# Kernel tuning notes

Measured on AMD Instinct MI355X. Metric: run time of the kernel, lower is better.

The kernel has to match this reference:

```python
import jax, jax.numpy as jnp
import numpy as np
import math

HEADS = 16
DIMS = 1024
SEQ_LEN = 2048
RANK_K = 128
BATCH = 8


def setup_inputs() -> dict:
    key = jax.random.key(0)
    ks = jax.random.split(key, 14)
    dh_std = 1.0 / math.sqrt(DIMS)
    proj_std = 1.0 / math.sqrt(RANK_K)
    inp = {
        "q": jax.random.normal(ks[0], (BATCH, SEQ_LEN, DIMS), jnp.float32),
        "k": jax.random.normal(ks[1], (BATCH, SEQ_LEN, DIMS), jnp.float32),
        "v": jax.random.normal(ks[2], (BATCH, SEQ_LEN, DIMS), jnp.float32),
        # nn.Linear weights [out, in], bias [out]
        "Wq": jax.random.uniform(ks[3], (DIMS, DIMS), jnp.float32, -dh_std, dh_std),
        "bq": jax.random.uniform(ks[4], (DIMS,), jnp.float32, -dh_std, dh_std),
        "Wk": jax.random.uniform(ks[5], (DIMS, DIMS), jnp.float32, -dh_std, dh_std),
        "bk": jax.random.uniform(ks[6], (DIMS,), jnp.float32, -dh_std, dh_std),
        "Wv": jax.random.uniform(ks[7], (DIMS, DIMS), jnp.float32, -dh_std, dh_std),
        "bv": jax.random.uniform(ks[8], (DIMS,), jnp.float32, -dh_std, dh_std),
        # Linformer low-rank projections [seq_length, k], uniform(-1/sqrt(k), 1/sqrt(k))
        "proj_k": jax.random.uniform(ks[9], (SEQ_LEN, RANK_K), jnp.float32, -proj_std, proj_std),
        "proj_v": jax.random.uniform(ks[10], (SEQ_LEN, RANK_K), jnp.float32, -proj_std, proj_std),
        "Wo": jax.random.uniform(ks[11], (DIMS, DIMS), jnp.float32, -dh_std, dh_std),
        "bo": jax.random.uniform(ks[12], (DIMS,), jnp.float32, -dh_std, dh_std),
    }
    return inp


def reference(q, k, v, Wq, bq, Wk, bk, Wv, bv, proj_k, proj_v, Wo, bo):
    B, N, D = q.shape
    H = HEADS
    dh = D // H
    Kr = proj_k.shape[1]

    kp = k @ Wk.T + bk                       # [B, N, D]
    # faithful to original: plain reshape (view), NOT a head-split transpose
    qp = (q @ Wq.T + bq).reshape(B, H, N, dh)  # [B, H, N, dh]
    vp = v @ Wv.T + bv                       # [B, N, D]

    pk = jnp.einsum('bnd,nk->bkd', kp, proj_k[:N])  # [B, Kr, D]
    pv = jnp.einsum('bnd,nk->bkd', vp, proj_v[:N])  # [B, Kr, D]
    pk = pk.reshape(B, Kr, H, dh).transpose(0, 2, 1, 3)  # [B, H, Kr, dh]
    pv = pv.reshape(B, Kr, H, dh).transpose(0, 2, 1, 3)  # [B, H, Kr, dh]

    # scores [B,H,N,Kr] -> transposed to [B,H,Kr,N]; softmax over N (seq) axis
    scores = jnp.einsum('bhnd,bhkd->bhkn', qp, pk) / math.sqrt(dh)
    attn = jax.nn.softmax(scores, axis=-1)   # [B, H, Kr, N]
    out = jnp.einsum('bhkn,bhkd->bhnd', attn, pv)  # [B, H, N, dh]
    out = out.transpose(0, 2, 1, 3).reshape(B, N, D)
    return out @ Wo.T + bo
```

## Files before the change

### kernel.cpp

```cpp
#include <hip/hip_runtime.h>

typedef unsigned short u16;
typedef unsigned int   u32;
typedef __attribute__((ext_vector_type(4))) float fx4;
typedef __attribute__((ext_vector_type(8))) __bf16 bf16x8;
typedef __attribute__((ext_vector_type(8))) unsigned short us8;
typedef __attribute__((ext_vector_type(2))) unsigned int u32x2;

__device__ __forceinline__ u16 f2bf(float x){
  u32 u = __builtin_bit_cast(u32, x);
  u += 0x7fffu + ((u >> 16) & 1u);
  return (u16)(u >> 16);
}
__device__ __forceinline__ float b2f(u16 h){
  u32 u = ((u32)h) << 16;
  return __builtin_bit_cast(float, u);
}
__device__ __forceinline__ void gld16(const void* g, void* l){
  __builtin_amdgcn_global_load_lds(
      (const __attribute__((address_space(1))) u32*)g,
      (__attribute__((address_space(3))) u32*)l, 16, 0, 0);
}
__device__ __forceinline__ void xcd_remap(u32& bx, u32& by, u32& bz){
  u32 nx = gridDim.x, ny = gridDim.y, nz = gridDim.z;
  u32 nwg = nx * ny * nz;
  u32 orig = (blockIdx.z * ny + blockIdx.y) * nx + blockIdx.x;
  u32 lid = (orig & 7u) * (nwg >> 3) + (orig >> 3);
  bx = lid % nx;
  u32 rem = lid / nx;
  by = rem % ny;
  bz = rem / ny;
}

__global__ __launch_bounds__(256) void k_f2bfAll(const float* __restrict__ w0,
                                                 const float* __restrict__ w1,
                                                 const float* __restrict__ w2,
                                                 const float* __restrict__ w3,
                                                 const float* __restrict__ q,
                                                 u16* __restrict__ wout,
                                                 u16* __restrict__ qout,
                                                 float* __restrict__ zbuf){
  if (blockIdx.x == 0 && blockIdx.y == 0) zbuf[threadIdx.x] = 0.f;
  const int y = blockIdx.y;
  const float* src;
  u16* dst;
  if (y < 4){
    src = y == 0 ? w0 : y == 1 ? w1 : y == 2 ? w2 : w3;
    dst = wout + (long)y * 1048576;
  } else {
    src = q + (long)(y - 4) * 1048576;
    dst = qout + (long)(y - 4) * 1048576;
  }
  int i = blockIdx.x * 256 + threadIdx.x;
  const int stride = gridDim.x * 256;
  for (; i < 131072; i += stride){
    const float4* p = (const float4*)src + (long)i * 2;
    float4 a = p[0], b = p[1];
    us8 o = { f2bf(a.x), f2bf(a.y), f2bf(a.z), f2bf(a.w),
              f2bf(b.x), f2bf(b.y), f2bf(b.z), f2bf(b.w) };
    *((us8*)dst + i) = o;
  }
}

__global__ __launch_bounds__(256) void k_tconvKV(const float* __restrict__ ksrc,
                                                 const float* __restrict__ vsrc,
                                                 u16* __restrict__ kT){
  const int z = blockIdx.z;
  const float* in = (z >= 8 ? vsrc : ksrc) + (long)(z & 7) * 2097152;
  u16* out = kT + (long)(z >> 3) * 16777216 + (long)(z & 7) * 2097152;
  const int c0 = blockIdx.x * 64, r0 = blockIdx.y * 64;
  __shared__ u16 tile[64][66];
  const int t = threadIdx.x;
  const int cc = t & 63, wq = t >> 6;
  #pragma unroll
  for (int i = 0; i < 16; ++i){
    int rr = i * 4 + wq;
    tile[rr][cc] = f2bf(in[(long)(r0 + rr) * 1024 + c0 + cc]);
  }
  __syncthreads();
  const int oc0 = t >> 5, jb = (t & 31) * 2;
  #pragma unroll
  for (int i = 0; i < 8; ++i){
    int oc = oc0 + i * 8;
    u32 pk2 = (u32)tile[jb][oc] | ((u32)tile[jb + 1][oc] << 16);
    *(u32*)(out + (long)(c0 + oc) * 2048 + r0 + jb) = pk2;
  }
}

__global__ __launch_bounds__(256) void k_tconvP(const float* __restrict__ pjk,
                                                const float* __restrict__ pjv,
                                                u16* __restrict__ projT,
                                                float* __restrict__ ssum){
  const int z = blockIdx.z;
  const float* in = z ? pjv : pjk;
  u16* out = projT + z * 262144;
  float* colsum = ssum + z * 128;
  const int c0 = blockIdx.x * 64, r0 = blockIdx.y * 64;
  __shared__ u16 tile[64][66];
  __shared__ float red[256];
  const int t = threadIdx.x;
  const int cc = t & 63, wq = t >> 6;
  float part = 0.f;
  #pragma unroll
  for (int i = 0; i < 16; ++i){
    int rr = i * 4 + wq;
    float v = in[(long)(r0 + rr) * 128 + c0 + cc];
    tile[rr][cc] = f2bf(v);
    part += v;
  }
  red[t] = part;
  __syncthreads();
  if (t < 64){
    float s = red[t] + red[t + 64] + red[t + 128] + red[t + 192];
    atomicAdd(&colsum[c0 + t], s);
  }
  __syncthreads();
  const int oc0 = t >> 5, jb = (t & 31) * 2;
  #pragma unroll
  for (int i = 0; i < 8; ++i){
    int oc = oc0 + i * 8;
    u32 pk2 = (u32)tile[jb][oc] | ((u32)tile[jb + 1][oc] << 16);
    *(u32*)(out + (long)(c0 + oc) * 2048 + r0 + jb) = pk2;
  }
}

template<int BM, int BN, int MODE, int EPI, typename OutT>
__global__ __launch_bounds__(256) void k_gemm(
    const u16* __restrict__ A, int lda, long sAz,
    const u16* __restrict__ B, int ldb, long sBz,
    OutT* __restrict__ C, int ldc, long sCz,
    int K, const float* __restrict__ bias, const float* __restrict__ srow, float scale)
{
  constexpr int BK = 64;
  constexpr int FM = BM / 32, FN = BN / 32;
  __shared__ u16 ldsA[BM * BK];
  __shared__ u16 ldsB[BN * BK];
  u32 bx, by, bz;
  xcd_remap(bx, by, bz);
  const long z = bz;
  if constexpr (MODE == 0){ A += z * sAz; B += z * sBz; C += z * sCz; }
  if constexpr (MODE == 3){ long p = z >> 3, bb = z & 7;
                            A += p * 262144; B += p * 16777216 + bb * 2097152;
                            C += p * 1048576 + bb * 131072; }
  const int t = threadIdx.x;
  const int lane = t & 63;
  const int w = t >> 6, wm = w >> 1, wn = w & 1;
  const int r15 = lane & 15, g = lane >> 4;
  const int m0 = by * BM, n0 = bx * BN;
  fx4 acc[FM][FN] = {};
  constexpr int CA = BM * BK / (8 * 256);
  constexpr int CB = BN * BK / (8 * 256);
  for (int kt = 0; kt < K; kt += BK){
    #pragma unroll
    for (int i = 0; i < CA; ++i){
      int ch = i * 256 + t, row = ch >> 3, cc = ch & 7;
      gld16(A + (long)(m0 + row) * lda + kt + cc * 8, (char*)ldsA + ch * 16);
    }
    #pragma unroll
    for (int i = 0; i < CB; ++i){
      int ch = i * 256 + t, row = ch >> 3, cc = ch & 7;
      gld16(B + (long)(n0 + row) * ldb + kt + cc * 8, (char*)ldsB + ch * 16);
    }
    __syncthreads();
    #pragma unroll
    for (int ks = 0; ks < 2; ++ks){
      bf16x8 af[FM], bfv[FN];
      #pragma unroll
      for (int mf = 0; mf < FM; ++mf)
        af[mf] = *(const bf16x8*)&ldsA[(wm * (BM/2) + mf * 16 + r15) * BK + ks * 32 + g * 8];
      #pragma unroll
      for (int nf = 0; nf < FN; ++nf)
        bfv[nf] = *(const bf16x8*)&ldsB[(wn * (BN/2) + nf * 16 + r15) * BK + ks * 32 + g * 8];
      #pragma unroll
      for (int mf = 0; mf < FM; ++mf)
        #pragma unroll
        for (int nf = 0; nf < FN; ++nf)
          acc[mf][nf] = __builtin_amdgcn_mfma_f32_16x16x32_bf16(af[mf], bfv[nf], acc[mf][nf], 0, 0, 0);
    }
    __syncthreads();
  }
  #pragma unroll
  for (int mf = 0; mf < FM; ++mf){
    #pragma unroll
    for (int nf = 0; nf < FN; ++nf){
      const int row0 = m0 + wm * (BM/2) + mf * 16 + g * 4;
      const int col  = n0 + wn * (BN/2) + nf * 16 + r15;
      float vv[4];
      #pragma unroll
      for (int r = 0; r < 4; ++r){
        float v = acc[mf][nf][r];
        if constexpr (EPI == 1) v += bias[col];
        vv[r] = v;
      }
      #pragma unroll
      for (int r = 0; r < 4; ++r){
        if constexpr (sizeof(OutT) == 2) C[(long)(row0 + r) * ldc + col] = (OutT)f2bf(vv[r]);
        else                             C[(long)(row0 + r) * ldc + col] = (OutT)vv[r];
      }
    }
  }
}

__global__ __launch_bounds__(256) void k_pkpv(
    const u16* __restrict__ ck, const u16* __restrict__ Wk_bf,
    const u16* __restrict__ Wv_bf, const float* __restrict__ bk,
    const float* __restrict__ bv, const float* __restrict__ ssum,
    u16* __restrict__ pk, u16* __restrict__ pvT)
{
  constexpr int BM = 64, BN = 64, BK = 64;
  __shared__ u16 ldsA[BM * BK];
  __shared__ u16 ldsB[BN * BK];
  u32 bx, by, bz;
  xcd_remap(bx, by, bz);
  const int half = bz >> 3, b = bz & 7;
  const u16* A = ck + half * 1048576 + b * 131072;
  const u16* B = half ? Wv_bf : Wk_bf;
  const float* bias = half ? bv : bk;
  const float* srow = ssum + half * 128;
  const float scale = half ? 1.f : 0.125f;
  const int t = threadIdx.x;
  const int lane = t & 63;
  const int w = t >> 6, wm = w >> 1, wn = w & 1;
  const int r15 = lane & 15, g = lane >> 4;
  const int m0 = by * BM, n0 = bx * BN;
  fx4 acc[2][2] = {};
  for (int kt = 0; kt < 1024; kt += BK){
    #pragma unroll
    for (int i = 0; i < 2; ++i){
      int ch = i * 256 + t, row = ch >> 3, cc = ch & 7;
      gld16(A + (long)(m0 + row) * 1024 + kt + cc * 8, (char*)ldsA + ch * 16);
    }
    #pragma unroll
    for (int i = 0; i < 2; ++i){
      int ch = i * 256 + t, row = ch >> 3, cc = ch & 7;
      gld16(B + (long)(n0 + row) * 1024 + kt + cc * 8, (char*)ldsB + ch * 16);
    }
    __syncthreads();
    #pragma unroll
    for (int ks = 0; ks < 2; ++ks){
      bf16x8 af[2], bfv[2];
      #pragma unroll
      for (int mf = 0; mf < 2; ++mf)
        af[mf] = *(const bf16x8*)&ldsA[(wm * 32 + mf * 16 + r15) * BK + ks * 32 + g * 8];
      #pragma unroll
      for (int nf = 0; nf < 2; ++nf)
        bfv[nf] = *(const bf16x8*)&ldsB[(wn * 32 + nf * 16 + r15) * BK + ks * 32 + g * 8];
      #pragma unroll
      for (int mf = 0; mf < 2; ++mf)
        #pragma unroll
        for (int nf = 0; nf < 2; ++nf)
          acc[mf][nf] = __builtin_amdgcn_mfma_f32_16x16x32_bf16(af[mf], bfv[nf], acc[mf][nf], 0, 0, 0);
    }
    __syncthreads();
  }
  #pragma unroll
  for (int mf = 0; mf < 2; ++mf){
    #pragma unroll
    for (int nf = 0; nf < 2; ++nf){
      const int row0 = m0 + wm * 32 + mf * 16 + g * 4;
      const int col  = n0 + wn * 32 + nf * 16 + r15;
      float vv[4];
      #pragma unroll
      for (int r = 0; r < 4; ++r)
        vv[r] = (acc[mf][nf][r] + srow[row0 + r] * bias[col]) * scale;
      if (!half){
        #pragma unroll
        for (int r = 0; r < 4; ++r)
          pk[b * 131072 + (long)(row0 + r) * 1024 + col] = f2bf(vv[r]);
      } else {
        u32 lo = (u32)f2bf(vv[0]) | ((u32)f2bf(vv[1]) << 16);
        u32 hi = (u32)f2bf(vv[2]) | ((u32)f2bf(vv[3]) << 16);
        u32x2 pk2 = { lo, hi };
        *(u32x2*)(pvT + b * 131072 + (long)col * 128 + row0) = pk2;
      }
    }
  }
}

template<int EPI, typename OutT>
__global__ __launch_bounds__(512, 1) void k_gemm256(
    const u16* __restrict__ A, int lda,
    const u16* __restrict__ B, int ldb,
    OutT* __restrict__ C, int ldc,
    int K, const float* __restrict__ bias)
{
  constexpr int BM = 256, BN = 128, BK = 64;
  __shared__ u16 ldsA[3][BM * BK];
  __shared__ u16 ldsB[3][BN * BK];
  u32 bx, by, bz;
  xcd_remap(bx, by, bz);
  const int m0 = by * BM, n0 = bx * BN;
  const int t = threadIdx.x;
  const int lane = t & 63, w = t >> 6;
  const int wm = w >> 1, wn = w & 1;
  const int r15 = lane & 15, g = lane >> 4;
  const int NT = K >> 6;

  auto stageA = [&](int kt, int buf){
    #pragma unroll
    for (int j = 0; j < 4; ++j){
      int ch = j * 512 + t, row = ch >> 3, cc = ch & 7;
      gld16(A + (long)(m0 + row) * lda + kt + ((cc ^ (row & 7)) * 8),
            (char*)ldsA[buf] + ch * 16);
    }
  };
  auto stageB = [&](int kt, int buf){
    #pragma unroll
    for (int j = 0; j < 2; ++j){
      int ch = j * 512 + t, row = ch >> 3, cc = ch & 7;
      gld16(B + (long)(n0 + row) * ldb + kt + ((cc ^ (row & 7)) * 8),
            (char*)ldsB[buf] + ch * 16);
    }
  };

  stageA(0, 0); stageB(0, 0);
  if (NT > 1){
    stageA(BK, 1); stageB(BK, 1);
    asm volatile("s_waitcnt vmcnt(6)" ::: "memory");
  } else {
    asm volatile("s_waitcnt vmcnt(0)" ::: "memory");
  }
  __builtin_amdgcn_s_barrier();
  asm volatile("" ::: "memory");

  fx4 acc[4][4] = {};
  for (int tt = 0; tt < NT; ++tt){
    const u16* bA = ldsA[tt % 3];
    const u16* bB = ldsB[tt % 3];
    const int sbuf = (tt + 2) % 3;
    const bool pf = (tt + 2 < NT);
    bf16x8 af[2][4], bf[2][2];
    #pragma unroll
    for (int ks = 0; ks < 2; ++ks)
      #pragma unroll
      for (int mf = 0; mf < 4; ++mf)
        af[ks][mf] = *(const bf16x8*)((const char*)bA +
            (wm * 64 + mf * 16 + r15) * 128 + (((ks * 4 + g) ^ (r15 & 7)) * 16));
    #pragma unroll
    for (int ks = 0; ks < 2; ++ks)
      #pragma unroll
      for (int nf = 0; nf < 2; ++nf)
        bf[ks][nf] = *(const bf16x8*)((const char*)bB +
            (wn * 64 + nf * 16 + r15) * 128 + (((ks * 4 + g) ^ (r15 & 7)) * 16));
    if (pf) stageA((tt + 2) * BK, sbuf);
    asm volatile("" ::: "memory");
    __builtin_amdgcn_s_barrier();
    asm volatile("" ::: "memory");
    __builtin_amdgcn_s_setprio(1);
    #pragma unroll
    for (int ks = 0; ks < 2; ++ks)
      #pragma unroll
      for (int mf = 0; mf < 4; ++mf)
        #pragma unroll
        for (int nf = 0; nf < 2; ++nf)
          acc[mf][nf] = __builtin_amdgcn_mfma_f32_16x16x32_bf16(af[ks][mf], bf[ks][nf], acc[mf][nf], 0, 0, 0);
    __builtin_amdgcn_s_setprio(0);
    asm volatile("" ::: "memory");
    __builtin_amdgcn_s_barrier();
    asm volatile("" ::: "memory");
    bf16x8 bf2[2][2];
    #pragma unroll
    for (int ks = 0; ks < 2; ++ks)
      #pragma unroll
      for (int nf = 0; nf < 2; ++nf)
        bf2[ks][nf] = *(const bf16x8*)((const char*)bB +
            (wn * 64 + (nf + 2) * 16 + r15) * 128 + (((ks * 4 + g) ^ (r15 & 7)) * 16));
    if (pf) stageB((tt + 2) * BK, sbuf);
    __builtin_amdgcn_s_setprio(1);
    #pragma unroll
    for (int ks = 0; ks < 2; ++ks)
      #pragma unroll
      for (int mf = 0; mf < 4; ++mf)
        #pragma unroll
        for (int nf = 0; nf < 2; ++nf)
          acc[mf][nf + 2] = __builtin_amdgcn_mfma_f32_16x16x32_bf16(af[ks][mf], bf2[ks][nf], acc[mf][nf + 2], 0, 0, 0);
    __builtin_amdgcn_s_setprio(0);
    if (pf)                { asm volatile("s_waitcnt vmcnt(6)" ::: "memory"); }
    else if (tt + 1 < NT)  { asm volatile("s_waitcnt vmcnt(0)" ::: "memory"); }
    asm volatile("" ::: "memory");
    __builtin_amdgcn_s_barrier();
    asm volatile("" ::: "memory");
  }

  #pragma unroll
  for (int mf = 0; mf < 4; ++mf)
    #pragma unroll
    for (int nf = 0; nf < 4; ++nf){
      const int row0 = m0 + wm * 64 + mf * 16 + g * 4;
      const int col  = n0 + wn * 64 + nf * 16 + r15;
      float bcol = 0.f;
      if constexpr (EPI == 1) bcol = bias[col];
      #pragma unroll
      for (int r = 0; r < 4; ++r){
        float vv = acc[mf][nf][r] + bcol;
        if constexpr (sizeof(OutT) == 2) C[(long)(row0 + r) * ldc + col] = (OutT)f2bf(vv);
        else                             C[(long)(row0 + r) * ldc + col] = (OutT)vv;
      }
    }
}

__global__ __launch_bounds__(512) void k_stats(const u16* __restrict__ pk,
                                               const u16* __restrict__ qp,
                                               float* __restrict__ zpart){
  const int hf = blockIdx.x, z = blockIdx.y;
  const int b = z >> 4, h = z & 15;
  const u16* pkh = pk + b * 131072 + h * 64;
  const u16* qph = qp + (long)z * 131072;
  __shared__ u16 pkL[128 * 64];
  __shared__ float zred[8][128];
  const int t = threadIdx.x, lane = t & 63, w = t >> 6;
  const int r15 = lane & 15, g = lane >> 4;
  #pragma unroll
  for (int i = 0; i < 2; ++i){
    int ch = i * 512 + t, row = ch >> 3, cc = ch & 7;
    int csrc = cc ^ (row & 7);
    gld16(pkh + (long)row * 1024 + csrc * 8, (char*)pkL + ch * 16);
  }
  __syncthreads();
  float zacc[8][4] = {};
  for (int c = 0; c < 4; ++c){
    const int n0 = hf * 1024 + w * 128 + c * 32;
    fx4 acc[8][2] = {};
    #pragma unroll
    for (int ks = 0; ks < 2; ++ks){
      bf16x8 bq[2];
      #pragma unroll
      for (int nf = 0; nf < 2; ++nf)
        bq[nf] = *(const bf16x8*)(qph + (long)(n0 + nf * 16 + r15) * 64 + ks * 32 + g * 8);
      #pragma unroll
      for (int mf = 0; mf < 8; ++mf){
        int row = mf * 16 + r15;
        int x = (ks * 4 + g) ^ (row & 7);
        bf16x8 a = *(const bf16x8*)((const char*)pkL + row * 128 + x * 16);
        #pragma unroll
        for (int nf = 0; nf < 2; ++nf)
          acc[mf][nf] = __builtin_amdgcn_mfma_f32_16x16x32_bf16(a, bq[nf], acc[mf][nf], 0, 0, 0);
      }
    }
    #pragma unroll
    for (int mf = 0; mf < 8; ++mf)
      #pragma unroll
      for (int nf = 0; nf < 2; ++nf)
        #pragma unroll
        for (int r = 0; r < 4; ++r)
          zacc[mf][r] += __expf(acc[mf][nf][r]);
  }
  #pragma unroll
  for (int mf = 0; mf < 8; ++mf)
    #pragma unroll
    for (int r = 0; r < 4; ++r){
      float v = zacc[mf][r];
      v += __shfl_xor(v, 1); v += __shfl_xor(v, 2);
      v += __shfl_xor(v, 4); v += __shfl_xor(v, 8);
      zacc[mf][r] = v;
    }
  if (r15 == 0){
    #pragma unroll
    for (int mf = 0; mf < 8; ++mf)
      #pragma unroll
      for (int r = 0; r < 4; ++r)
        zred[w][mf * 16 + g * 4 + r] = zacc[mf][r];
  }
  __syncthreads();
  if (t < 128){
    float s = 0.f;
    #pragma unroll
    for (int w2 = 0; w2 < 8; ++w2) s += zred[w2][t];
    zpart[hf * 16384 + (long)z * 128 + t] = s;
  }
}

__global__ __launch_bounds__(256) void k_attn(const u16* __restrict__ pk,
                                              const u16* __restrict__ qp,
                                              const u16* __restrict__ pvT,
                                              const float* __restrict__ zpart,
                                              u16* __restrict__ outh){
  u32 bx, by, bz;
  xcd_remap(bx, by, bz);
  const int z = by, nb = bx;
  const int b = z >> 4, h = z & 15;
  const u16* pkh = pk  + b * 131072 + h * 64;
  const u16* qph = qp  + (long)z * 131072;
  const u16* pvh = pvT + b * 131072 + h * 8192;
  __shared__ u16 pkL[128 * 64];
  __shared__ u16 ptL[4][32 * 132];
  __shared__ float zL[128];
  const int t = threadIdx.x, lane = t & 63, w = t >> 6;
  const int r15 = lane & 15, g = lane >> 4;
  #pragma unroll
  for (int i = 0; i < 4; ++i){
    int ch = i * 256 + t, row = ch >> 3, cc = ch & 7;
    int csrc = cc ^ (row & 7);
    gld16(pkh + (long)row * 1024 + csrc * 8, (char*)pkL + ch * 16);
  }
  if (t < 128)
    zL[t] = 1.0f / (zpart[(long)z * 128 + t] + zpart[16384 + (long)z * 128 + t]);
  __syncthreads();
  const int n0 = nb * 128 + w * 32;
  fx4 acc[8][2] = {};
  #pragma unroll
  for (int ks = 0; ks < 2; ++ks){
    bf16x8 bq[2];
    #pragma unroll
    for (int nf = 0; nf < 2; ++nf)
      bq[nf] = *(const bf16x8*)(qph + (long)(n0 + nf * 16 + r15) * 64 + ks * 32 + g * 8);
    #pragma unroll
    for (int mf = 0; mf < 8; ++mf){
      int row = mf * 16 + r15;
      int x = (ks * 4 + g) ^ (row & 7);
      bf16x8 a = *(const bf16x8*)((const char*)pkL + row * 128 + x * 16);
      #pragma unroll
      for (int nf = 0; nf < 2; ++nf)
        acc[mf][nf] = __builtin_amdgcn_mfma_f32_16x16x32_bf16(a, bq[nf], acc[mf][nf], 0, 0, 0);
    }
  }
  u16* pt = ptL[w];
  #pragma unroll
  for (int mf = 0; mf < 8; ++mf){
    const int kb = mf * 16 + g * 4;
    const float z0 = zL[kb], z1 = zL[kb + 1], z2 = zL[kb + 2], z3 = zL[kb + 3];
    #pragma unroll
    for (int nf = 0; nf < 2; ++nf){
      const int nl = nf * 16 + r15;
      u32 lo = (u32)f2bf(__expf(acc[mf][nf][0]) * z0) |
               ((u32)f2bf(__expf(acc[mf][nf][1]) * z1) << 16);
      u32 hi = (u32)f2bf(__expf(acc[mf][nf][2]) * z2) |
               ((u32)f2bf(__expf(acc[mf][nf][3]) * z3) << 16);
      u32x2 pkd = { lo, hi };
      *(u32x2*)(pt + nl * 132 + kb) = pkd;
    }
  }
  fx4 o[2][4] = {};
  #pragma unroll
  for (int ks = 0; ks < 4; ++ks){
    bf16x8 bv[4];
    #pragma unroll
    for (int nf = 0; nf < 4; ++nf)
      bv[nf] = *(const bf16x8*)(pvh + (long)(nf * 16 + r15) * 128 + ks * 32 + g * 8);
    #pragma unroll
    for (int mf = 0; mf < 2; ++mf){
      bf16x8 pa = *(const bf16x8*)(pt + (mf * 16 + r15) * 132 + ks * 32 + g * 8);
      #pragma unroll
      for (int nf = 0; nf < 4; ++nf)
        o[mf][nf] = __builtin_amdgcn_mfma_f32_16x16x32_bf16(pa, bv[nf], o[mf][nf], 0, 0, 0);
    }
  }
  u16* og = outh + ((long)b * 2048 + n0) * 1024 + h * 64;
  #pragma unroll
  for (int mf = 0; mf < 2; ++mf)
    #pragma unroll
    for (int nf = 0; nf < 4; ++nf)
      #pragma unroll
      for (int r = 0; r < 4; ++r){
        int nl = mf * 16 + g * 4 + r;
        og[(long)nl * 1024 + nf * 16 + r15] = f2bf(o[mf][nf][r]);
      }
}

extern "C" void kernel_launch(void* const* d_in, const int* in_sizes, int n_in,
                              void* d_out, int out_size, void* d_ws, size_t ws_size,
                              hipStream_t stream)
{
  const float* q   = (const float*)d_in[0];
  const float* k   = (const float*)d_in[1];
  const float* v   = (const float*)d_in[2];
  const float* Wq  = (const float*)d_in[3];
  const float* bq  = (const float*)d_in[4];
  const float* Wk  = (const float*)d_in[5];
  const float* bk  = (const float*)d_in[6];
  const float* Wv  = (const float*)d_in[7];
  const float* bv  = (const float*)d_in[8];
  const float* pjk = (const float*)d_in[9];
  const float* pjv = (const float*)d_in[10];
  const float* Wo  = (const float*)d_in[11];
  const float* bo  = (const float*)d_in[12];

  if (ws_size < 152044544u) return;

  char* ws = (char*)d_ws;
  u16*  q_bf  = (u16*)(ws + 0);
  u16*  kT    = (u16*)(ws + 33554432);
  u16*  vT    = (u16*)(ws + 67108864);
  u16*  W_bf  = (u16*)(ws + 100663296);
  u16*  projT = (u16*)(ws + 109051904);
  float* sk   = (float*)(ws + 110100480);
  u16*  qp    = (u16*)(ws + 110101504);
  u16*  ck    = (u16*)(ws + 143655936);
  u16*  pk    = (u16*)(ws + 147850240);
  u16*  pvT   = (u16*)(ws + 149947392);
  float* zpart = (float*)(ws + 33554432);
  u16*  outh  = (u16*)(ws + 0);
  u16*  Wq_bf = W_bf, *Wk_bf = W_bf + 1048576, *Wv_bf = W_bf + 2097152, *Wo_bf = W_bf + 3145728;

  k_f2bfAll<<<dim3(128,20), 256, 0, stream>>>(Wq, Wk, Wv, Wo, q, W_bf, q_bf, sk);
  k_tconvP<<<dim3(2,32,2), 256, 0, stream>>>(pjk, pjv, projT, sk);
  k_tconvKV<<<dim3(16,32,16), 256, 0, stream>>>(k, v, kT);

  k_gemm256<1,u16><<<dim3(8,64), 512, 0, stream>>>(
      q_bf,1024, Wq_bf,1024, qp,1024, 1024, bq);
  k_gemm<128,64,3,0,u16><<<dim3(16,1,16), 256, 0, stream>>>(
      projT,2048,0, kT,2048,0, ck,1024,0, 2048, nullptr, nullptr, 1.f);
  k_pkpv<<<dim3(16,2,16), 256, 0, stream>>>(ck, Wk_bf, Wv_bf, bk, bv, sk, pk, pvT);
  k_stats<<<dim3(2,128), 512, 0, stream>>>(pk, qp, zpart);
  k_attn<<<dim3(16,128), 256, 0, stream>>>(pk, qp, pvT, zpart, outh);
  k_gemm256<1,float><<<dim3(8,64), 512, 0, stream>>>(
      outh,1024, Wo_bf,1024, (float*)d_out,1024, 1024, bo);
}
```

Measured before the change: 263.8 us.

## Enlarge GEMM tile to 256x256 with double-buffered staggered LDS staging

```diff
diff --git a/kernel.cpp b/kernel.cpp
--- a/kernel.cpp
+++ b/kernel.cpp
@@ -278,74 +278,84 @@
 }
 
 template<int EPI, typename OutT>
-__global__ __launch_bounds__(512, 1) void k_gemm256(
+__global__ __launch_bounds__(512, 1) void k_gemm256b(
     const u16* __restrict__ A, int lda,
     const u16* __restrict__ B, int ldb,
     OutT* __restrict__ C, int ldc,
     int K, const float* __restrict__ bias)
 {
-  constexpr int BM = 256, BN = 128, BK = 64;
-  __shared__ u16 ldsA[3][BM * BK];
-  __shared__ u16 ldsB[3][BN * BK];
+  constexpr int BM = 256, BN = 256, BK = 64;
+  __shared__ u16 ldsA[2][BM * BK];
+  __shared__ u16 ldsB[2][BN * BK];
   u32 bx, by, bz;
   xcd_remap(bx, by, bz);
   const int m0 = by * BM, n0 = bx * BN;
-  const int t = threadIdx.x;
-  const int lane = t & 63, w = t >> 6;
-  const int wm = w >> 1, wn = w & 1;
+  const int t = threadIdx.x, lane = t & 63, w = t >> 6;
+  const int wm = w >> 2, wn = w & 3;
   const int r15 = lane & 15, g = lane >> 4;
   const int NT = K >> 6;
 
-  auto stageA = [&](int kt, int buf){
-    #pragma unroll
-    for (int j = 0; j < 4; ++j){
-      int ch = j * 512 + t, row = ch >> 3, cc = ch & 7;
-      gld16(A + (long)(m0 + row) * lda + kt + ((cc ^ (row & 7)) * 8),
-            (char*)ldsA[buf] + ch * 16);
-    }
-  };
-  auto stageB = [&](int kt, int buf){
+  auto stA = [&](int buf, int half, int kt){
     #pragma unroll
     for (int j = 0; j < 2; ++j){
       int ch = j * 512 + t, row = ch >> 3, cc = ch & 7;
-      gld16(B + (long)(n0 + row) * ldb + kt + ((cc ^ (row & 7)) * 8),
-            (char*)ldsB[buf] + ch * 16);
+      gld16(A + (long)(m0 + half * 128 + row) * lda + kt + ((cc ^ (row & 7)) * 8),
+            (char*)ldsA[buf] + half * 16384 + ch * 16);
     }
   };
-
-  stageA(0, 0); stageB(0, 0);
-  if (NT > 1){
-    stageA(BK, 1); stageB(BK, 1);
-    asm volatile("s_waitcnt vmcnt(6)" ::: "memory");
-  } else {
-    asm volatile("s_waitcnt vmcnt(0)" ::: "memory");
-  }
+  auto stB = [&](int buf, int half, int kt){
+    #pragma unroll
+    for (int j = 0; j < 2; ++j){
+      int ch = j * 512 + t, row = ch >> 3, cc = ch & 7;
+      gld16(B + (long)(n0 + half * 128 + row) * ldb + kt + ((cc ^ (row & 7)) * 8),
+            (char*)ldsB[buf] + half * 16384 + ch * 16);
+    }
+  };
+
+  stB(0,0,0); stB(0,1,0); stA(0,0,0); stA(0,1,0);
+  if (NT > 1){ stB(1,0,BK); stB(1,1,BK); stA(1,0,BK); }
+  asm volatile("s_waitcnt vmcnt(6)" ::: "memory");
   __builtin_amdgcn_s_barrier();
   asm volatile("" ::: "memory");
 
-  fx4 acc[4][4] = {};
+  fx4 acc[8][4] = {};
   for (int tt = 0; tt < NT; ++tt){
-    const u16* bA = ldsA[tt % 3];
-    const u16* bB = ldsB[tt % 3];
-    const int sbuf = (tt + 2) % 3;
-    const bool pf = (tt + 2 < NT);
-    bf16x8 af[2][4], bf[2][2];
+    const int buf = tt & 1;
+    bf16x8 a[2][4], b01[2][2], b23[2][2];
+    #pragma unroll
+    for (int ks = 0; ks < 2; ++ks)
+      #pragma unroll
+      for (int mf = 0; mf < 4; ++mf){
+        int row = wm * 128 + mf * 16 + r15;
+        a[ks][mf] = *(const bf16x8*)((const char*)ldsA[buf] + row * 128 + (((ks*4+g) ^ (r15 & 7)) * 16));
+      }
+    #pragma unroll
+    for (int ks = 0; ks < 2; ++ks)
+      #pragma unroll
+      for (int nf = 0; nf < 2; ++nf){
+        int row = wn * 64 + nf * 16 + r15;
+        b01[ks][nf] = *(const bf16x8*)((const char*)ldsB[buf] + row * 128 + (((ks*4+g) ^ (r15 & 7)) * 16));
+      }
+    if (tt + 1 < NT) stA(buf ^ 1, 1, (tt + 1) * BK);
+    __builtin_amdgcn_s_setprio(1);
     #pragma unroll
     for (int ks = 0; ks < 2; ++ks)
       #pragma unroll
       for (int mf = 0; mf < 4; ++mf)
-        af[ks][mf] = *(const bf16x8*)((const char*)bA +
-            (wm * 64 + mf * 16 + r15) * 128 + (((ks * 4 + g) ^ (r15 & 7)) * 16));
-    #pragma unroll
-    for (int ks = 0; ks < 2; ++ks)
-      #pragma unroll
-      for (int nf = 0; nf < 2; ++nf)
-        bf[ks][nf] = *(const bf16x8*)((const char*)bB +
-            (wn * 64 + nf * 16 + r15) * 128 + (((ks * 4 + g) ^ (r15 & 7)) * 16));
-    if (pf) stageA((tt + 2) * BK, sbuf);
+        #pragma unroll
+        for (int nf = 0; nf < 2; ++nf)
+          acc[mf][nf] = __builtin_amdgcn_mfma_f32_16x16x32_bf16(a[ks][mf], b01[ks][nf], acc[mf][nf], 0, 0, 0);
+    __builtin_amdgcn_s_setprio(0);
     asm volatile("" ::: "memory");
     __builtin_amdgcn_s_barrier();
     asm volatile("" ::: "memory");
+    #pragma unroll
+    for (int ks = 0; ks < 2; ++ks)
+      #pragma unroll
+      for (int nf = 0; nf < 2; ++nf){
+        int row = wn * 64 + (nf + 2) * 16 + r15;
+        b23[ks][nf] = *(const bf16x8*)((const char*)ldsB[buf] + row * 128 + (((ks*4+g) ^ (r15 & 7)) * 16));
+      }
     __builtin_amdgcn_s_setprio(1);
     #pragma unroll
     for (int ks = 0; ks < 2; ++ks)
@@ -353,19 +363,19 @@
       for (int mf = 0; mf < 4; ++mf)
         #pragma unroll
         for (int nf = 0; nf < 2; ++nf)
-          acc[mf][nf] = __builtin_amdgcn_mfma_f32_16x16x32_bf16(af[ks][mf], bf[ks][nf], acc[mf][nf], 0, 0, 0);
+          acc[mf][nf + 2] = __builtin_amdgcn_mfma_f32_16x16x32_bf16(a[ks][mf], b23[ks][nf], acc[mf][nf + 2], 0, 0, 0);
     __builtin_amdgcn_s_setprio(0);
     asm volatile("" ::: "memory");
     __builtin_amdgcn_s_barrier();
     asm volatile("" ::: "memory");
-    bf16x8 bf2[2][2];
-    #pragma unroll
-    for (int ks = 0; ks < 2; ++ks)
-      #pragma unroll
-      for (int nf = 0; nf < 2; ++nf)
-        bf2[ks][nf] = *(const bf16x8*)((const char*)bB +
-            (wn * 64 + (nf + 2) * 16 + r15) * 128 + (((ks * 4 + g) ^ (r15 & 7)) * 16));
-    if (pf) stageB((tt + 2) * BK, sbuf);
+    #pragma unroll
+    for (int ks = 0; ks < 2; ++ks)
+      #pragma unroll
+      for (int mf = 0; mf < 4; ++mf){
+        int row = wm * 128 + (mf + 4) * 16 + r15;
+        a[ks][mf] = *(const bf16x8*)((const char*)ldsA[buf] + row * 128 + (((ks*4+g) ^ (r15 & 7)) * 16));
+      }
+    if (tt + 2 < NT) stB(buf, 0, (tt + 2) * BK);
     __builtin_amdgcn_s_setprio(1);
     #pragma unroll
     for (int ks = 0; ks < 2; ++ks)
@@ -373,20 +383,33 @@
       for (int mf = 0; mf < 4; ++mf)
         #pragma unroll
         for (int nf = 0; nf < 2; ++nf)
-          acc[mf][nf + 2] = __builtin_amdgcn_mfma_f32_16x16x32_bf16(af[ks][mf], bf2[ks][nf], acc[mf][nf + 2], 0, 0, 0);
+          acc[mf + 4][nf + 2] = __builtin_amdgcn_mfma_f32_16x16x32_bf16(a[ks][mf], b23[ks][nf], acc[mf + 4][nf + 2], 0, 0, 0);
     __builtin_amdgcn_s_setprio(0);
-    if (pf)                { asm volatile("s_waitcnt vmcnt(6)" ::: "memory"); }
-    else if (tt + 1 < NT)  { asm volatile("s_waitcnt vmcnt(0)" ::: "memory"); }
     asm volatile("" ::: "memory");
     __builtin_amdgcn_s_barrier();
     asm volatile("" ::: "memory");
-  }
-
-  #pragma unroll
-  for (int mf = 0; mf < 4; ++mf)
+    if (tt + 2 < NT){ stA(buf, 0, (tt + 2) * BK); stB(buf, 1, (tt + 2) * BK); }
+    __builtin_amdgcn_s_setprio(1);
+    #pragma unroll
+    for (int ks = 0; ks < 2; ++ks)
+      #pragma unroll
+      for (int mf = 0; mf < 4; ++mf)
+        #pragma unroll
+        for (int nf = 0; nf < 2; ++nf)
+          acc[mf + 4][nf] = __builtin_amdgcn_mfma_f32_16x16x32_bf16(a[ks][mf], b01[ks][nf], acc[mf + 4][nf], 0, 0, 0);
+    __builtin_amdgcn_s_setprio(0);
+    if (tt + 2 < NT)      { asm volatile("s_waitcnt vmcnt(6)" ::: "memory"); }
+    else if (tt + 1 < NT) { asm volatile("s_waitcnt vmcnt(0)" ::: "memory"); }
+    asm volatile("" ::: "memory");
+    __builtin_amdgcn_s_barrier();
+    asm volatile("" ::: "memory");
+  }
+
+  #pragma unroll
+  for (int mf = 0; mf < 8; ++mf)
     #pragma unroll
     for (int nf = 0; nf < 4; ++nf){
-      const int row0 = m0 + wm * 64 + mf * 16 + g * 4;
+      const int row0 = m0 + wm * 128 + mf * 16 + g * 4;
       const int col  = n0 + wn * 64 + nf * 16 + r15;
       float bcol = 0.f;
       if constexpr (EPI == 1) bcol = bias[col];
@@ -596,13 +619,13 @@
   k_tconvP<<<dim3(2,32,2), 256, 0, stream>>>(pjk, pjv, projT, sk);
   k_tconvKV<<<dim3(16,32,16), 256, 0, stream>>>(k, v, kT);
 
-  k_gemm256<1,u16><<<dim3(8,64), 512, 0, stream>>>(
+  k_gemm256b<1,u16><<<dim3(4,64), 512, 0, stream>>>(
       q_bf,1024, Wq_bf,1024, qp,1024, 1024, bq);
   k_gemm<128,64,3,0,u16><<<dim3(16,1,16), 256, 0, stream>>>(
       projT,2048,0, kT,2048,0, ck,1024,0, 2048, nullptr, nullptr, 1.f);
   k_pkpv<<<dim3(16,2,16), 256, 0, stream>>>(ck, Wk_bf, Wv_bf, bk, bv, sk, pk, pvT);
   k_stats<<<dim3(2,128), 512, 0, stream>>>(pk, qp, zpart);
   k_attn<<<dim3(16,128), 256, 0, stream>>>(pk, qp, pvT, zpart, outh);
-  k_gemm256<1,float><<<dim3(8,64), 512, 0, stream>>>(
+  k_gemm256b<1,float><<<dim3(4,64), 512, 0, stream>>>(
       outh,1024, Wo_bf,1024, (float*)d_out,1024, 1024, bo);
 }
```

Result: no change. 266.8 us (+1.1%).
